# Kernel optimization log

Measured on AMD Instinct MI355X. Metric: run time of the kernel, lower is better.

Reference implementation:

```python
import jax, jax.numpy as jnp
import numpy as np
from jax import lax

INPLANES = 512
PLANES = 512
MID = PLANES // 4  # expansion = 4
G = 4              # patch_groups
EPS = 1e-5


def _conv(x, w, groups, pad):
    return lax.conv_general_dilated(
        x, w, window_strides=(1, 1), padding=[(pad, pad), (pad, pad)],
        dimension_numbers=('NCHW', 'OIHW', 'NCHW'), feature_group_count=groups)


def _bn(x, gamma, beta, mean, var):
    scale = gamma / jnp.sqrt(var + EPS)
    return x * scale[None, :, None, None] + (beta - mean * scale)[None, :, None, None]


def _upmask(mask, c, h, w):
    # [b,g,mh,mw] -> repeat each group over c//g channels (group-major channel order),
    # then nearest-upsample to (h, w) (exact integer repeat, matches F.interpolate nearest)
    b, g, mh, mw = mask.shape
    m = jnp.repeat(mask, c // g, axis=1)
    m = jnp.repeat(m, h // mh, axis=2)
    m = jnp.repeat(m, w // mw, axis=3)
    return m


def setup_inputs() -> dict:
    key = jax.random.key(0)
    ks = jax.random.split(key, 20)
    x = jax.random.normal(ks[0], (16, INPLANES, 56, 56), dtype=jnp.float32)
    mask = jax.random.randint(ks[1], (16, G, 7, 7), 0, 2).astype(jnp.float32)
    s = 0.05
    w1 = jax.random.normal(ks[2], (MID, INPLANES // G, 1, 1), dtype=jnp.float32) * s
    w2 = jax.random.normal(ks[3], (MID, MID // G, 3, 3), dtype=jnp.float32) * s
    w3 = jax.random.normal(ks[4], (PLANES, MID // G, 1, 1), dtype=jnp.float32) * s
    def bnp(k, c):
        k1, k2, k3, k4 = jax.random.split(k, 4)
        return (jax.random.normal(k1, (c,), jnp.float32) * 0.1 + 1.0,  # gamma
                jax.random.normal(k2, (c,), jnp.float32) * 0.1,        # beta
                jax.random.normal(k3, (c,), jnp.float32) * 0.1,        # running mean
                jax.random.uniform(k4, (c,), jnp.float32, 0.5, 1.5))   # running var
    g1, b1, m1, v1 = bnp(ks[5], MID)
    g2, b2, m2, v2 = bnp(ks[6], MID)
    g3, b3, m3, v3 = bnp(ks[7], PLANES)
    return dict(x=x, mask=mask, w1=w1, g1=g1, b1=b1, m1=m1, v1=v1,
                w2=w2, g2=g2, b2=b2, m2=m2, v2=v2,
                w3=w3, g3=g3, b3=b3, m3=m3, v3=v3)


def reference(x, mask, w1, g1, b1, m1, v1, w2, g2, b2, m2, v2, w3, g3, b3, m3, v3):
    b, c, h, w = x.shape
    residual = x
    mask1 = _upmask(mask, c, h, w)           # [b, c, h, w]
    out = x * mask1
    out = jax.nn.relu(_bn(_conv(out, w1, G, 0), g1, b1, m1, v1))  # [b, MID, h, w]
    mask2 = _upmask(mask, out.shape[1], h, w)
    out = out * mask2
    out = jax.nn.relu(_bn(_conv(out, w2, G, 1), g2, b2, m2, v2))
    out = out * mask2
    out = _bn(_conv(out, w3, G, 0), g3, b3, m3, v3)
    out = out + residual
    return jax.nn.relu(out)
```

## Files before the change

kernel.cpp:

```cpp
#include <hip/hip_runtime.h>
#include <stdint.h>

typedef unsigned short U16;
typedef unsigned int   U32;
typedef __attribute__((ext_vector_type(8))) short short8;
typedef __attribute__((ext_vector_type(4))) float floatx4;

#define HW 3136
#define ICS 40

__device__ __forceinline__ U16 f2b(float f){
    union { float f; unsigned int i; } v; v.f = f;
    unsigned int u = (v.i + 0x7FFFu + ((v.i >> 16) & 1u)) >> 16;
    return (U16)u;
}
__device__ __forceinline__ short8 pack8(const float* p){
    float4 a = *reinterpret_cast<const float4*>(p);
    float4 b = *reinterpret_cast<const float4*>(p + 4);
    short8 r;
    r[0]=(short)f2b(a.x); r[1]=(short)f2b(a.y); r[2]=(short)f2b(a.z); r[3]=(short)f2b(a.w);
    r[4]=(short)f2b(b.x); r[5]=(short)f2b(b.y); r[6]=(short)f2b(b.z); r[7]=(short)f2b(b.w);
    return r;
}

__global__ void k_pre(const float* __restrict__ w2,
                      const float* g1, const float* b1, const float* m1, const float* v1,
                      const float* g2, const float* b2, const float* m2, const float* v2,
                      const float* g3, const float* b3, const float* m3, const float* v3,
                      U16* __restrict__ w2t, float* __restrict__ bn){
  int i = blockIdx.x * 256 + threadIdx.x;
  if (i < 4*9*32*32) {
    int ic  = i & 31;
    int oc  = (i >> 5) & 31;
    int gt  = i >> 10;
    int g_  = gt / 9, tap = gt % 9;
    w2t[i] = f2b(w2[((g_*32 + oc)*32 + ic)*9 + tap]);
  } else {
    int j = i - 4*9*32*32;
    if (j >= 768) return;
    const float *gp, *bp, *mp, *vp; int c, so, sho;
    if (j < 128)      { c = j;       gp=g1; bp=b1; mp=m1; vp=v1; so = 0;   sho = 128;  }
    else if (j < 256) { c = j - 128; gp=g2; bp=b2; mp=m2; vp=v2; so = 256; sho = 384;  }
    else              { c = j - 256; gp=g3; bp=b3; mp=m3; vp=v3; so = 512; sho = 1024; }
    float s = gp[c] / sqrtf(vp[c] + 1e-5f);
    bn[so + c]  = s;
    bn[sho + c] = bp[c] - mp[c] * s;
  }
}

__global__ __launch_bounds__(512) void k_conv1(const float* __restrict__ x,
        const float* __restrict__ mask, const float* __restrict__ w1,
        const float* __restrict__ bn, U16* __restrict__ t1){
  const int t = threadIdx.x;
  const int lane = t & 63, wave = t >> 6;
  const int quad = lane >> 4, l15 = lane & 15;
  const int oct = wave & 1, pxq = wave >> 1;
  const int b = blockIdx.z, g = blockIdx.y, mh = blockIdx.x;
  const int h0 = mh*8, wbase = pxq*112;
  __shared__ float mk[7];
  __shared__ __align__(16) U16 xs[32*460];
  if (t < 7) mk[t] = mask[((b*4 + g)*7 + mh)*7 + t];
  const float* xg = x + (size_t)(b*512 + g*128)*HW + h0*56;
  U16* t1g = t1 + ((size_t)(b*4 + g)*HW + h0*56)*32;

  const float* wg = w1 + (size_t)(g*32)*128;
  short8 afr[4];
  #pragma unroll
  for (int ks = 0; ks < 4; ++ks)
    afr[ks] = pack8(wg + (oct*16 + l15)*128 + ks*32 + quad*8);

  floatx4 acc[7] = {};
  #pragma unroll
  for (int ch = 0; ch < 4; ++ch){
    __syncthreads();
    #pragma unroll
    for (int k = 0; k < 7; ++k){
      int idx = k*512 + t;
      int ic = idx / 112, f = idx - ic*112;
      int px = f*4;
      float4 v = *reinterpret_cast<const float4*>(xg + (size_t)(ch*32 + ic)*HW + px);
      float m = mk[(px % 56) >> 3];
      U32 lo = (U32)f2b(v.x*m) | ((U32)f2b(v.y*m) << 16);
      U32 hi = (U32)f2b(v.z*m) | ((U32)f2b(v.w*m) << 16);
      *reinterpret_cast<uint2*>(&xs[ic*460 + px]) = make_uint2(lo, hi);
    }
    __syncthreads();
    #pragma unroll
    for (int pxt = 0; pxt < 7; ++pxt){
      short8 bfr;
      #pragma unroll
      for (int j = 0; j < 8; ++j)
        bfr[j] = (short)xs[(quad*8 + j)*460 + wbase + pxt*16 + l15];
      acc[pxt] = __builtin_amdgcn_mfma_f32_16x16x32_bf16(afr[ch], bfr, acc[pxt], 0,0,0);
    }
  }
  const float* scp = bn + g*32 + oct*16 + quad*4;
  const float* shp = scp + 128;
  #pragma unroll
  for (int pxt = 0; pxt < 7; ++pxt){
    int px = wbase + pxt*16 + l15;
    float m = mk[(px % 56) >> 3];
    U16 y[4];
    #pragma unroll
    for (int reg = 0; reg < 4; ++reg)
      y[reg] = f2b(fmaxf(scp[reg]*acc[pxt][reg] + shp[reg], 0.0f) * m);
    *reinterpret_cast<uint2*>(t1g + (size_t)px*32 + oct*16 + quad*4) =
        make_uint2((U32)y[0] | ((U32)y[1]<<16), (U32)y[2] | ((U32)y[3]<<16));
  }
}

__global__ __launch_bounds__(512) void k_conv23(const U16* __restrict__ t1,
        const float* __restrict__ mask, const U16* __restrict__ w2t,
        const float* __restrict__ w3, const float* __restrict__ bn,
        const float* __restrict__ x, float* __restrict__ out){
  const int t = threadIdx.x;
  const int lane = t & 63, wave = t >> 6;
  const int quad = lane >> 4, l15 = lane & 15;
  const int b = blockIdx.z, g = blockIdx.y, mh = blockIdx.x;
  const int h0 = mh*8;
  __shared__ float mk[7];
  __shared__ __align__(16) U16 s[580*ICS];
  U16* t2s = s;
  if (t < 7) mk[t] = mask[((b*4 + g)*7 + mh)*7 + t];
  if (t < 80){
    int si = t >> 2, part = t & 3;
    int r = si >> 1, side = si & 1;
    *reinterpret_cast<uint4*>(&s[(r*58 + (side ? 57 : 0))*ICS + part*8]) =
        make_uint4(0,0,0,0);
  }
  const U16* tg = t1 + (size_t)(b*4 + g)*HW*32;
  #pragma unroll
  for (int k = 0; k < 5; ++k){
    int idx = k*512 + t;
    if (idx < 2240){
      int part = idx & 3, pxi = idx >> 2;
      int r = pxi / 56, c = pxi - r*56;
      int hh = h0 - 1 + r;
      uint4 v = make_uint4(0,0,0,0);
      if ((unsigned)hh < 56u)
        v = *reinterpret_cast<const uint4*>(tg + (size_t)(hh*56 + c)*32 + part*8);
      *reinterpret_cast<uint4*>(&s[(r*58 + c + 1)*ICS + part*8]) = v;
    }
  }
  __syncthreads();

  const int oct = wave & 1, rq = wave >> 1;
  floatx4 acc[7] = {};
  {
    const U16* wg = w2t + g*9*32*32;
    #pragma unroll
    for (int kh = 0; kh < 3; ++kh){
      const int lr = rq*2 + (l15 >> 3) + kh;
      #pragma unroll
      for (int kw = 0; kw < 3; ++kw){
        int tap = kh*3 + kw;
        short8 a0 = *reinterpret_cast<const short8*>(wg + (tap*32 + oct*16 + l15)*32 + quad*8);
        #pragma unroll
        for (int pxt = 0; pxt < 7; ++pxt){
          int cslot = pxt*8 + (l15 & 7) + kw;
          short8 bfr = *reinterpret_cast<const short8*>(
              &s[(lr*58 + cslot)*ICS + quad*8]);
          acc[pxt] = __builtin_amdgcn_mfma_f32_16x16x32_bf16(a0, bfr, acc[pxt], 0,0,0);
        }
      }
    }
  }
  __syncthreads();

  {
    const int pr = rq*2 + (l15 >> 3);
    const float* scp = bn + 256 + g*32 + oct*16 + quad*4;
    const float* shp = bn + 384 + g*32 + oct*16 + quad*4;
    #pragma unroll
    for (int pxt = 0; pxt < 7; ++pxt){
      float m = mk[pxt];
      U16 y[4];
      #pragma unroll
      for (int reg = 0; reg < 4; ++reg)
        y[reg] = f2b(fmaxf(scp[reg]*acc[pxt][reg] + shp[reg], 0.0f) * m);
      int px = pr*56 + pxt*8 + (l15 & 7);
      *reinterpret_cast<uint2*>(&t2s[px*ICS + oct*16 + quad*4]) =
          make_uint2((U32)y[0] | ((U32)y[1]<<16), (U32)y[2] | ((U32)y[3]<<16));
    }
  }
  __syncthreads();

  {
    short8 afr = pack8(w3 + (size_t)(g*128 + wave*16 + l15)*32 + quad*8);
    const float* scp = bn + 512 + g*128 + wave*16 + quad*4;
    const float* shp = bn + 1024 + g*128 + wave*16 + quad*4;
    const float* xg = x + (size_t)(b*512 + g*128)*HW + h0*56;
    float* og = out + (size_t)(b*512 + g*128)*HW + h0*56;
    #pragma unroll
    for (int tt = 0; tt < 28; ++tt){
      int px = tt*16 + l15;
      short8 bfr = *reinterpret_cast<const short8*>(&t2s[px*ICS + quad*8]);
      floatx4 acc3 = {};
      acc3 = __builtin_amdgcn_mfma_f32_16x16x32_bf16(afr, bfr, acc3, 0,0,0);
      #pragma unroll
      for (int reg = 0; reg < 4; ++reg){
        size_t o2 = (size_t)(wave*16 + quad*4 + reg)*HW + px;
        og[o2] = fmaxf(scp[reg]*acc3[reg] + shp[reg] + xg[o2], 0.0f);
      }
    }
  }
}

extern "C" void kernel_launch(void* const* d_in, const int* in_sizes, int n_in,
                              void* d_out, int out_size, void* d_ws, size_t ws_size,
                              hipStream_t stream){
  const float* x    = (const float*)d_in[0];
  const float* mask = (const float*)d_in[1];
  const float* w1   = (const float*)d_in[2];
  const float* g1   = (const float*)d_in[3];
  const float* b1   = (const float*)d_in[4];
  const float* m1   = (const float*)d_in[5];
  const float* v1   = (const float*)d_in[6];
  const float* w2   = (const float*)d_in[7];
  const float* g2   = (const float*)d_in[8];
  const float* b2   = (const float*)d_in[9];
  const float* m2   = (const float*)d_in[10];
  const float* v2   = (const float*)d_in[11];
  const float* w3   = (const float*)d_in[12];
  const float* g3   = (const float*)d_in[13];
  const float* b3   = (const float*)d_in[14];
  const float* m3   = (const float*)d_in[15];
  const float* v3   = (const float*)d_in[16];

  char* ws = (char*)d_ws;
  U16*   w2t = (U16*)ws;
  float* bn  = (float*)(ws + 73728);
  U16*   t1  = (U16*)(ws + 79872);

  k_pre<<<147, 256, 0, stream>>>(w2, g1,b1,m1,v1, g2,b2,m2,v2, g3,b3,m3,v3, w2t, bn);
  dim3 grid(7, 4, 16);
  k_conv1<<<grid, 512, 0, stream>>>(x, mask, w1, bn, t1);
  k_conv23<<<grid, 512, 0, stream>>>(t1, mask, w2t, w3, bn, x, (float*)d_out);
}
```

Measured before the change: 275.8 us.

## Fuse prep into conv1, skip masked loads and MFMAs, nontemporal residual I/O

Drops the separate preprocessing kernel. Its weight transpose and BN folding now run in one extra block of the conv1 grid, and conv1 computes its own BN1 scale and shift locally. Loads of x and t1 are skipped for masked-out 8x8 patches, and conv2 MFMAs are skipped for masked column tiles, cutting memory traffic and compute in proportion to mask sparsity. The residual read and output write use nontemporal hints. Running the whole prep inside a single block may serialize that work, and the skip branches add divergence.

```diff
diff --git a/kernel.cpp b/kernel.cpp
--- a/kernel.cpp
+++ b/kernel.cpp
@@ -23,43 +23,53 @@
     return r;
 }
 
-__global__ void k_pre(const float* __restrict__ w2,
-                      const float* g1, const float* b1, const float* m1, const float* v1,
-                      const float* g2, const float* b2, const float* m2, const float* v2,
-                      const float* g3, const float* b3, const float* m3, const float* v3,
-                      U16* __restrict__ w2t, float* __restrict__ bn){
-  int i = blockIdx.x * 256 + threadIdx.x;
-  if (i < 4*9*32*32) {
-    int ic  = i & 31;
-    int oc  = (i >> 5) & 31;
-    int gt  = i >> 10;
-    int g_  = gt / 9, tap = gt % 9;
-    w2t[i] = f2b(w2[((g_*32 + oc)*32 + ic)*9 + tap]);
-  } else {
-    int j = i - 4*9*32*32;
-    if (j >= 768) return;
-    const float *gp, *bp, *mp, *vp; int c, so, sho;
-    if (j < 128)      { c = j;       gp=g1; bp=b1; mp=m1; vp=v1; so = 0;   sho = 128;  }
-    else if (j < 256) { c = j - 128; gp=g2; bp=b2; mp=m2; vp=v2; so = 256; sho = 384;  }
-    else              { c = j - 256; gp=g3; bp=b3; mp=m3; vp=v3; so = 512; sho = 1024; }
-    float s = gp[c] / sqrtf(vp[c] + 1e-5f);
-    bn[so + c]  = s;
-    bn[sho + c] = bp[c] - mp[c] * s;
-  }
-}
-
 __global__ __launch_bounds__(512) void k_conv1(const float* __restrict__ x,
         const float* __restrict__ mask, const float* __restrict__ w1,
-        const float* __restrict__ bn, U16* __restrict__ t1){
+        const float* __restrict__ w2,
+        const float* g1, const float* b1, const float* m1, const float* v1,
+        const float* g2, const float* b2, const float* m2, const float* v2,
+        const float* g3, const float* b3, const float* m3, const float* v3,
+        U16* __restrict__ w2t, float* __restrict__ bn, U16* __restrict__ t1){
   const int t = threadIdx.x;
+  const int b = blockIdx.z, g = blockIdx.y, mh = blockIdx.x;
+
+  if (mh == 7){
+    if ((g | b) != 0) return;
+    for (int i = t; i < 4*9*32*32 + 768; i += 512){
+      if (i < 4*9*32*32){
+        int ic  = i & 31;
+        int oc  = (i >> 5) & 31;
+        int gt  = i >> 10;
+        int g_  = gt / 9, tap = gt % 9;
+        w2t[i] = f2b(w2[((g_*32 + oc)*32 + ic)*9 + tap]);
+      } else {
+        int j = i - 4*9*32*32;
+        const float *gp, *bp, *mp, *vp; int c, so, sho;
+        if (j < 128)      { c = j;       gp=g1; bp=b1; mp=m1; vp=v1; so = 0;   sho = 128;  }
+        else if (j < 256) { c = j - 128; gp=g2; bp=b2; mp=m2; vp=v2; so = 256; sho = 384;  }
+        else              { c = j - 256; gp=g3; bp=b3; mp=m3; vp=v3; so = 512; sho = 1024; }
+        float s = gp[c] / sqrtf(vp[c] + 1e-5f);
+        bn[so + c]  = s;
+        bn[sho + c] = bp[c] - mp[c] * s;
+      }
+    }
+    return;
+  }
+
   const int lane = t & 63, wave = t >> 6;
   const int quad = lane >> 4, l15 = lane & 15;
   const int oct = wave & 1, pxq = wave >> 1;
-  const int b = blockIdx.z, g = blockIdx.y, mh = blockIdx.x;
   const int h0 = mh*8, wbase = pxq*112;
   __shared__ float mk[7];
+  __shared__ float bnl[64];
   __shared__ __align__(16) U16 xs[32*460];
   if (t < 7) mk[t] = mask[((b*4 + g)*7 + mh)*7 + t];
+  if (t < 32){
+    int c = g*32 + t;
+    float s = g1[c] / sqrtf(v1[c] + 1e-5f);
+    bnl[t]      = s;
+    bnl[32 + t] = b1[c] - m1[c] * s;
+  }
   const float* xg = x + (size_t)(b*512 + g*128)*HW + h0*56;
   U16* t1g = t1 + ((size_t)(b*4 + g)*HW + h0*56)*32;
 
@@ -78,11 +88,14 @@
       int idx = k*512 + t;
       int ic = idx / 112, f = idx - ic*112;
       int px = f*4;
-      float4 v = *reinterpret_cast<const float4*>(xg + (size_t)(ch*32 + ic)*HW + px);
       float m = mk[(px % 56) >> 3];
-      U32 lo = (U32)f2b(v.x*m) | ((U32)f2b(v.y*m) << 16);
-      U32 hi = (U32)f2b(v.z*m) | ((U32)f2b(v.w*m) << 16);
-      *reinterpret_cast<uint2*>(&xs[ic*460 + px]) = make_uint2(lo, hi);
+      uint2 pk = make_uint2(0u, 0u);
+      if (m != 0.0f){
+        float4 v = *reinterpret_cast<const float4*>(xg + (size_t)(ch*32 + ic)*HW + px);
+        pk.x = (U32)f2b(v.x*m) | ((U32)f2b(v.y*m) << 16);
+        pk.y = (U32)f2b(v.z*m) | ((U32)f2b(v.w*m) << 16);
+      }
+      *reinterpret_cast<uint2*>(&xs[ic*460 + px]) = pk;
     }
     __syncthreads();
     #pragma unroll
@@ -94,8 +107,8 @@
       acc[pxt] = __builtin_amdgcn_mfma_f32_16x16x32_bf16(afr[ch], bfr, acc[pxt], 0,0,0);
     }
   }
-  const float* scp = bn + g*32 + oct*16 + quad*4;
-  const float* shp = scp + 128;
+  const float* scp = bnl + oct*16 + quad*4;
+  const float* shp = scp + 32;
   #pragma unroll
   for (int pxt = 0; pxt < 7; ++pxt){
     int px = wbase + pxt*16 + l15;
@@ -121,7 +134,8 @@
   __shared__ float mk[7];
   __shared__ __align__(16) U16 s[580*ICS];
   U16* t2s = s;
-  if (t < 7) mk[t] = mask[((b*4 + g)*7 + mh)*7 + t];
+  const float* mg = mask + (b*4 + g)*49;
+  if (t < 7) mk[t] = mg[mh*7 + t];
   if (t < 80){
     int si = t >> 2, part = t & 3;
     int r = si >> 1, side = si & 1;
@@ -137,12 +151,15 @@
       int r = pxi / 56, c = pxi - r*56;
       int hh = h0 - 1 + r;
       uint4 v = make_uint4(0,0,0,0);
-      if ((unsigned)hh < 56u)
+      if ((unsigned)hh < 56u && mg[(hh>>3)*7 + (c>>3)] != 0.0f)
         v = *reinterpret_cast<const uint4*>(tg + (size_t)(hh*56 + c)*32 + part*8);
       *reinterpret_cast<uint4*>(&s[(r*58 + c + 1)*ICS + part*8]) = v;
     }
   }
   __syncthreads();
+  float mkr[7];
+  #pragma unroll
+  for (int i = 0; i < 7; ++i) mkr[i] = mk[i];
 
   const int oct = wave & 1, rq = wave >> 1;
   floatx4 acc[7] = {};
@@ -157,6 +174,7 @@
         short8 a0 = *reinterpret_cast<const short8*>(wg + (tap*32 + oct*16 + l15)*32 + quad*8);
         #pragma unroll
         for (int pxt = 0; pxt < 7; ++pxt){
+          if (mkr[pxt] == 0.0f) continue;
           int cslot = pxt*8 + (l15 & 7) + kw;
           short8 bfr = *reinterpret_cast<const short8*>(
               &s[(lr*58 + cslot)*ICS + quad*8]);
@@ -173,7 +191,7 @@
     const float* shp = bn + 384 + g*32 + oct*16 + quad*4;
     #pragma unroll
     for (int pxt = 0; pxt < 7; ++pxt){
-      float m = mk[pxt];
+      float m = mkr[pxt];
       U16 y[4];
       #pragma unroll
       for (int reg = 0; reg < 4; ++reg)
@@ -200,7 +218,9 @@
       #pragma unroll
       for (int reg = 0; reg < 4; ++reg){
         size_t o2 = (size_t)(wave*16 + quad*4 + reg)*HW + px;
-        og[o2] = fmaxf(scp[reg]*acc3[reg] + shp[reg] + xg[o2], 0.0f);
+        float xr = __builtin_nontemporal_load(&xg[o2]);
+        __builtin_nontemporal_store(
+            fmaxf(scp[reg]*acc3[reg] + shp[reg] + xr, 0.0f), &og[o2]);
       }
     }
   }
@@ -232,8 +252,9 @@
   float* bn  = (float*)(ws + 73728);
   U16*   t1  = (U16*)(ws + 79872);
 
-  k_pre<<<147, 256, 0, stream>>>(w2, g1,b1,m1,v1, g2,b2,m2,v2, g3,b3,m3,v3, w2t, bn);
-  dim3 grid(7, 4, 16);
-  k_conv1<<<grid, 512, 0, stream>>>(x, mask, w1, bn, t1);
-  k_conv23<<<grid, 512, 0, stream>>>(t1, mask, w2t, w3, bn, x, (float*)d_out);
-}
+  dim3 grid1(8, 4, 16);
+  k_conv1<<<grid1, 512, 0, stream>>>(x, mask, w1, w2,
+      g1,b1,m1,v1, g2,b2,m2,v2, g3,b3,m3,v3, w2t, bn, t1);
+  dim3 grid2(7, 4, 16);
+  k_conv23<<<grid2, 512, 0, stream>>>(t1, mask, w2t, w3, bn, x, (float*)d_out);
+}
```

Result: slower. 299.4 us (+8.5%).
